# Kernel tuning notes

Hardware: AMD Instinct MI355X
Metric: run time of the kernel (lower is better)

Reference implementation:

```python
import jax, jax.numpy as jnp
import numpy as np

DECAY = 0.99
EPS = 1e-05


def setup_inputs() -> dict:
    key = jax.random.key(0)
    k1, k2, k3, k4 = jax.random.split(key, 4)
    x = jax.random.normal(k1, (32, 64, 64, 64), jnp.float32)          # [B,H,W,dim]
    embed = jax.random.normal(k2, (64, 1024), jnp.float32)            # [dim, n_embed] buffer
    cluster_size = jax.random.uniform(k3, (1024,), jnp.float32)       # EMA cluster-size buffer
    embed_avg = jax.random.normal(k4, (64, 1024), jnp.float32)        # EMA embed-avg buffer
    return {"x": x, "embed": embed, "cluster_size": cluster_size, "embed_avg": embed_avg}


def reference(x, embed, cluster_size, embed_avg):
    dim = x.shape[-1]
    n_embed = embed.shape[1]
    flatten = x.reshape(-1, dim)                                      # [N, dim]
    # squared distances: ||f||^2 - 2 f.E + ||e||^2   -> [N, n_embed]
    dist = ((flatten * flatten).sum(1, keepdims=True)
            - 2.0 * (flatten @ embed)
            + (embed * embed).sum(0, keepdims=True))
    idx = jnp.argmin(dist, axis=1)                                    # [N]
    quantize = jnp.take(embed.T, idx, axis=0).reshape(x.shape)        # codebook gather
    embed_ind = idx.reshape(x.shape[:-1])

    # EMA codebook update (training branch); stats detached as in torch (buffers, .data ops)
    fl = jax.lax.stop_gradient(flatten)
    onehot_sum = jax.ops.segment_sum(jnp.ones_like(idx, dtype=x.dtype), idx, num_segments=n_embed)
    embed_sum = jax.ops.segment_sum(fl, idx, num_segments=n_embed).T  # [dim, n_embed]
    new_cluster_size = DECAY * cluster_size + (1.0 - DECAY) * onehot_sum
    new_embed_avg = DECAY * embed_avg + (1.0 - DECAY) * embed_sum
    n = new_cluster_size.sum()
    cs = (new_cluster_size + EPS) / (n + n_embed * EPS) * n
    new_embed = new_embed_avg / cs[None, :]

    diff = jnp.mean((jax.lax.stop_gradient(quantize) - x) ** 2)       # commitment loss
    quantize_st = x + jax.lax.stop_gradient(quantize - x)             # straight-through
    return (quantize_st, diff, embed_ind, new_cluster_size, new_embed_avg, new_embed)
```

## Files before the change

kernel.cpp:

```cpp
#include <hip/hip_runtime.h>


#define N_ROWS 131072
#define DIM    64
#define NEMB   1024
#define NRANGE 32
#define KMASK  0xFFFFFC00u
#define TAUK   0.05f

static constexpr float DECAYF = 0.99f;
static constexpr float OMDF   = (float)(1.0 - 0.99);
static constexpr float EPSF   = 1e-5f;
static constexpr float NEPSF  = (float)(1024 * 1e-5);

typedef __attribute__((ext_vector_type(8))) short short8;
typedef __attribute__((ext_vector_type(4))) float f32x4;

static __device__ __forceinline__ unsigned short f2bf(float f) {
    unsigned int u = __builtin_bit_cast(unsigned int, f);
    unsigned int r = (u + 0x7FFFu + ((u >> 16) & 1u)) >> 16;
    return (unsigned short)r;
}
static __device__ __forceinline__ float bf2f(unsigned short h) {
    unsigned int u = ((unsigned int)h) << 16;
    return __builtin_bit_cast(float, u);
}

#define WS_ESUM    0
#define WS_CNTF    65536
#define WS_DIFF    66560
#define WS_FLAGCNT 66561
#define WS_N       66562
#define WS_EE      66564
#define WS_EMBEDT  67588
#define WS_IDX     133124
#define WS_FLAGLST 264196
#define WS_BFRAG   395268
#define WS_CNTPART 460804
#define WS_PART    493572
#define WS_NEED_BYTES ((size_t)(WS_PART + NRANGE * 65536) * 4)

__global__ void prep_kernel(const float* __restrict__ embed,
                            float* __restrict__ embedT,
                            float* __restrict__ ee,
                            uint4* __restrict__ BfragG,
                            float* __restrict__ ws_diff) {
    int tid = blockIdx.x * 256 + threadIdx.x;
    if (tid == 0) ws_diff[0] = 0.f;
    for (int i = 0; i < 4; ++i) {
        int id = i * 16384 + tid;
        int d = id >> 10, e = id & 1023;
        embedT[e * 64 + d] = embed[id];
    }
    if (tid < NEMB) {
        float s = 0.f;
        for (int d = 0; d < DIM; ++d) {
            float v = embed[d * 1024 + tid];
            s = fmaf(v, v, s);
        }
        ee[tid] = s;
    }
    int fid  = tid >> 6;
    int lane = tid & 63;
    int hl = fid & 1, kt = (fid >> 1) & 1, ct = fid >> 2;
    int col = ct * 16 + (lane & 15);
    int k0  = kt * 32 + (lane >> 4) * 8;
    unsigned short u[8];
    #pragma unroll
    for (int j = 0; j < 8; ++j) {
        float v = -2.0f * embed[(k0 + j) * 1024 + col];
        unsigned short h = f2bf(v);
        if (hl) h = f2bf(v - bf2f(h));
        u[j] = h;
    }
    uint4 wv;
    wv.x = (unsigned)u[0] | ((unsigned)u[1] << 16);
    wv.y = (unsigned)u[2] | ((unsigned)u[3] << 16);
    wv.z = (unsigned)u[4] | ((unsigned)u[5] << 16);
    wv.w = (unsigned)u[6] | ((unsigned)u[7] << 16);
    BfragG[fid * 64 + lane] = wv;
}

__global__ __launch_bounds__(256) void dist_kernel(
        const float* __restrict__ x, const uint4* __restrict__ BfragG,
        const float* __restrict__ ee, const float* __restrict__ embed,
        const float* __restrict__ embedT,
        float* __restrict__ out_q, float* __restrict__ out_ind,
        int* __restrict__ ws_idx, float* __restrict__ ws_diff) {
    __shared__ float sEE[1024];
    __shared__ int   sIdx[128];
    __shared__ float red[4];
    __shared__ int   sFlagCnt;
    __shared__ int   sFlagRows[128];
    __shared__ float sx[8][64];
    __shared__ float sff[8];
    __shared__ float sbdw[8][4];
    __shared__ int   sbiw[8][4];
    __shared__ int   schg[8];

    const int t = threadIdx.x;
    const int w = t >> 6, lane = t & 63;
    const int quad = lane >> 4, wl = lane & 15;
    const int rbase = blockIdx.x * 128;

    short8 a_hi[2][2], a_lo[2][2];
    #pragma unroll
    for (int rt = 0; rt < 2; ++rt) {
        int row = rbase + w * 32 + rt * 16 + wl;
        #pragma unroll
        for (int kt = 0; kt < 2; ++kt) {
            const float* px = x + (size_t)row * 64 + kt * 32 + quad * 8;
            float4 v0 = *(const float4*)px;
            float4 v1 = *(const float4*)(px + 4);
            float vv[8] = {v0.x, v0.y, v0.z, v0.w, v1.x, v1.y, v1.z, v1.w};
            short8 ah, al;
            #pragma unroll
            for (int j = 0; j < 8; ++j) {
                unsigned short h = f2bf(vv[j]);
                ah[j] = (short)h;
                al[j] = (short)f2bf(vv[j] - bf2f(h));
            }
            a_hi[rt][kt] = ah; a_lo[rt][kt] = al;
        }
    }

    for (int i = t; i < 1024; i += 256) sEE[i] = ee[i];
    if (t == 0) sFlagCnt = 0;

    float b1[8], b2[8];
    #pragma unroll
    for (int s = 0; s < 8; ++s) { b1[s] = 3.4e38f; b2[s] = 3.4e38f; }

    const f32x4 zacc = {0.f, 0.f, 0.f, 0.f};

    __syncthreads();

#define GBODY(CB0, CB1, CB2, CB3, COLV)                                        \
    {                                                                          \
        short8 bh0 = __builtin_bit_cast(short8, CB0);                          \
        short8 bl0 = __builtin_bit_cast(short8, CB1);                          \
        short8 bh1 = __builtin_bit_cast(short8, CB2);                          \
        short8 bl1 = __builtin_bit_cast(short8, CB3);                          \
        float eec = sEE[COLV];                                                 \
        unsigned colu = (unsigned)(COLV);                                      \
        _Pragma("unroll")                                                      \
        for (int rt = 0; rt < 2; ++rt) {                                       \
            f32x4 c0 = __builtin_amdgcn_mfma_f32_16x16x32_bf16(a_lo[rt][0], bh0, zacc, 0, 0, 0); \
            f32x4 c1 = __builtin_amdgcn_mfma_f32_16x16x32_bf16(a_lo[rt][1], bh1, zacc, 0, 0, 0); \
            c0 = __builtin_amdgcn_mfma_f32_16x16x32_bf16(a_hi[rt][0], bl0, c0, 0, 0, 0); \
            c1 = __builtin_amdgcn_mfma_f32_16x16x32_bf16(a_hi[rt][1], bl1, c1, 0, 0, 0); \
            c0 = __builtin_amdgcn_mfma_f32_16x16x32_bf16(a_hi[rt][0], bh0, c0, 0, 0, 0); \
            c1 = __builtin_amdgcn_mfma_f32_16x16x32_bf16(a_hi[rt][1], bh1, c1, 0, 0, 0); \
            _Pragma("unroll")                                                  \
            for (int reg = 0; reg < 4; ++reg) {                                \
                float s = c0[reg] + c1[reg] + eec;                             \
                unsigned ku = ((__builtin_bit_cast(unsigned, s) + 0x200u) & KMASK) | colu; \
                float key = __builtin_bit_cast(float, ku);                     \
                int st = rt * 4 + reg;                                         \
                b2[st] = __builtin_amdgcn_fmed3f(key, b1[st], b2[st]);         \
                b1[st] = fminf(key, b1[st]);                                   \
            }                                                                  \
        }                                                                      \
    }

#define LOADB(S0, S1, S2, S3, P)                                               \
    { const uint4* _p = (P); S0 = _p[0]; S1 = _p[64]; S2 = _p[128]; S3 = _p[192]; }

    {
        const uint4* pa = BfragG + lane;
        uint4 A0, A1, A2, A3, B0, B1, B2, B3;
        uint4 C0, C1, C2, C3, D0, D1, D2, D3;
        LOADB(A0, A1, A2, A3, pa);
        LOADB(B0, B1, B2, B3, pa + 256);
        LOADB(C0, C1, C2, C3, pa + 512);
        LOADB(D0, D1, D2, D3, pa + 768);
        int col = wl;
        for (int it = 0; it < 64; it += 4) {
            GBODY(A0, A1, A2, A3, col);
            if (it + 4 < 64) LOADB(A0, A1, A2, A3, pa + (it + 4) * 256);
            GBODY(B0, B1, B2, B3, col + 16);
            if (it + 5 < 64) LOADB(B0, B1, B2, B3, pa + (it + 5) * 256);
            GBODY(C0, C1, C2, C3, col + 32);
            if (it + 6 < 64) LOADB(C0, C1, C2, C3, pa + (it + 6) * 256);
            GBODY(D0, D1, D2, D3, col + 48);
            if (it + 7 < 64) LOADB(D0, D1, D2, D3, pa + (it + 7) * 256);
            col += 64;
        }
    }
#undef GBODY
#undef LOADB

    for (int m = 1; m < 16; m <<= 1) {
        #pragma unroll
        for (int s = 0; s < 8; ++s) {
            float o1 = __shfl_xor(b1[s], m);
            float o2 = __shfl_xor(b2[s], m);
            float mx = fmaxf(b1[s], o1);
            b1[s] = fminf(b1[s], o1);
            b2[s] = fminf(fminf(b2[s], o2), mx);
        }
    }
    if (wl == 0) {
        #pragma unroll
        for (int s = 0; s < 8; ++s) {
            int rt = s >> 2, reg = s & 3;
            int rloc = w * 32 + rt * 16 + quad * 4 + reg;
            int row = rbase + rloc;
            unsigned kb = __builtin_bit_cast(unsigned, b1[s]);
            int col = (int)(kb & 1023u);
            sIdx[rloc] = col;
            ws_idx[row] = col;
            out_ind[row] = (float)col;
            float v1 = __builtin_bit_cast(float, kb & KMASK);
            float v2 = __builtin_bit_cast(float, __builtin_bit_cast(unsigned, b2[s]) & KMASK);
            if (v2 - v1 < TAUK) {
                int p = atomicAdd(&sFlagCnt, 1);
                sFlagRows[p] = rloc;
            }
        }
    }
    __syncthreads();

    {
        int r = t >> 1, hh = t & 1;
        int e = sIdx[r];
        const float4* et = (const float4*)(embedT + e * 64 + hh * 32);
        const float4* xr = (const float4*)(x + (size_t)(rbase + r) * 64 + hh * 32);
        float4*       qo = (float4*)(out_q + (size_t)(rbase + r) * 64 + hh * 32);
        float dsum = 0.f;
        #pragma unroll
        for (int v = 0; v < 8; ++v) {
            float4 q4 = et[v];
            float4 x4 = xr[v];
            float dx = q4.x - x4.x, dy = q4.y - x4.y, dz = q4.z - x4.z, dw = q4.w - x4.w;
            float4 o;
            o.x = x4.x + dx; o.y = x4.y + dy; o.z = x4.z + dz; o.w = x4.w + dw;
            qo[v] = o;
            dsum += dx * dx + dy * dy + dz * dz + dw * dw;
        }
        for (int o2 = 32; o2 > 0; o2 >>= 1) dsum += __shfl_down(dsum, o2);
        if (lane == 0) red[w] = dsum;
        __syncthreads();
        if (t == 0) atomicAdd(ws_diff, red[0] + red[1] + red[2] + red[3]);
    }

    __syncthreads();
    int fcnt = sFlagCnt;
    for (int base = 0; base < fcnt; base += 8) {
        int nr = fcnt - base; if (nr > 8) nr = 8;
        __syncthreads();
        for (int l = t; l < nr * 64; l += 256) {
            int rl = sFlagRows[base + (l >> 6)];
            sx[l >> 6][l & 63] = x[(size_t)(rbase + rl) * 64 + (l & 63)];
        }
        __syncthreads();
        if (t < nr) {
            float ff = 0.f;
            for (int k = 0; k < 64; ++k) ff = fmaf(sx[t][k], sx[t][k], ff);
            sff[t] = ff;
        }
        float acc[8][4];
        #pragma unroll
        for (int r = 0; r < 8; ++r)
            #pragma unroll
            for (int j = 0; j < 4; ++j) acc[r][j] = 0.f;
        int c0i = t * 4;
        for (int k = 0; k < 64; ++k) {
            float4 e4 = *(const float4*)(embed + k * 1024 + c0i);
            #pragma unroll
            for (int r = 0; r < 8; ++r) {
                float xk = sx[r][k];
                acc[r][0] = fmaf(xk, e4.x, acc[r][0]);
                acc[r][1] = fmaf(xk, e4.y, acc[r][1]);
                acc[r][2] = fmaf(xk, e4.z, acc[r][2]);
                acc[r][3] = fmaf(xk, e4.w, acc[r][3]);
            }
        }
        __syncthreads();
        #pragma unroll
        for (int r = 0; r < 8; ++r) {
            if (r < nr) {
                float ff = sff[r];
                float bd = 3.4e38f; int bi = 0;
                #pragma unroll
                for (int j = 0; j < 4; ++j) {
                    float d = (ff - 2.f * acc[r][j]) + sEE[c0i + j];
                    if (d < bd) { bd = d; bi = c0i + j; }
                }
                for (int m = 32; m > 0; m >>= 1) {
                    float od = __shfl_xor(bd, m);
                    int   oi = __shfl_xor(bi, m);
                    if (od < bd || (od == bd && oi < bi)) { bd = od; bi = oi; }
                }
                if (lane == 0) { sbdw[r][w] = bd; sbiw[r][w] = bi; }
            }
        }
        __syncthreads();
        if (t < nr) {
            float bd = sbdw[t][0]; int bi = sbiw[t][0];
            #pragma unroll
            for (int k2 = 1; k2 < 4; ++k2) {
                float od = sbdw[t][k2]; int oi = sbiw[t][k2];
                if (od < bd || (od == bd && oi < bi)) { bd = od; bi = oi; }
            }
            int rl = sFlagRows[base + t];
            int oi_ = sIdx[rl];
            schg[t] = (bi != oi_) ? bi : -1;
            if (bi != oi_) {
                ws_idx[rbase + rl] = bi;
                out_ind[rbase + rl] = (float)bi;
            }
        }
        __syncthreads();
        for (int r = w; r < nr; r += 4) {
            int ni = schg[r];
            if (ni >= 0) {
                int rl = sFlagRows[base + r];
                int row = rbase + rl;
                int oi_ = sIdx[rl];
                float xv = sx[r][lane];
                float dn   = embedT[ni * 64 + lane] - xv;
                float dold = embedT[oi_ * 64 + lane] - xv;
                out_q[(size_t)row * 64 + lane] = xv + dn;
                float delta = dn * dn - dold * dold;
                for (int o = 32; o > 0; o >>= 1) delta += __shfl_down(delta, o);
                if (lane == 0) atomicAdd(ws_diff, delta);
            }
        }
    }
}

__global__ __launch_bounds__(1024) void scatter_kernel(
        const int* __restrict__ idx, const float* __restrict__ x,
        float* __restrict__ part_or_esum, float* __restrict__ cntp_or_cntf,
        int use_atomic) {
    __shared__ float shist[8192];
    __shared__ float scnt[1024];
    const int t = threadIdx.x;
    const int bid = blockIdx.x;
    const int oct = (bid >> 3) & 7;
    const int rb  = (bid & 7) | ((bid >> 6) << 3);
    const int sid = rb * 8 + oct;
    const int w = t >> 6, lane = t & 63;
    const int g = lane >> 3, d = lane & 7;

    for (int i = t; i < 8192; i += 1024) shist[i] = 0.f;
    if (oct == 0) { if (t < 1024) scnt[t] = 0.f; }
    __syncthreads();

    const int row0 = rb * 4096 + w * 256;
    int rcur = row0 + g;
    int e_n = idx[rcur];
    float x_n = x[(size_t)rcur * 64 + oct * 8 + d];
    for (int it = 0; it < 32; ++it) {
        int e = e_n; float xv = x_n;
        int rnext = rcur + 8;
        if (it < 31) {
            e_n = idx[rnext];
            x_n = x[(size_t)rnext * 64 + oct * 8 + d];
        }
        rcur = rnext;
        atomicAdd(&shist[e * 8 + d], xv);
        if (oct == 0 && d == 0) atomicAdd(&scnt[e], 1.0f);
    }
    __syncthreads();

    if (!use_atomic) {
        float* dst = part_or_esum + (size_t)sid * 8192;
        for (int out = t; out < 8192; out += 1024)
            dst[out] = shist[(out & 1023) * 8 + (out >> 10)];
        if (oct == 0) {
            float* cdst = cntp_or_cntf + rb * 1024;
            if (t < 1024) cdst[t] = scnt[t];
        }
    } else {
        for (int out = t; out < 8192; out += 1024) {
            float v = shist[(out & 1023) * 8 + (out >> 10)];
            if (v != 0.f)
                atomicAdd(&part_or_esum[(oct * 8 + (out >> 10)) * 1024 + (out & 1023)], v);
        }
        if (oct == 0) {
            if (t < 1024) {
                float c = scnt[t];
                if (c != 0.f) atomicAdd(&cntp_or_cntf[t], c);
            }
        }
    }
}

__global__ __launch_bounds__(1024) void finalizeF(
        const float* __restrict__ cluster_size, const float* __restrict__ cntp,
        const float* __restrict__ part, int nrb,
        const float* __restrict__ ws_diff, const float* __restrict__ embed_avg,
        float* __restrict__ out_diff, float* __restrict__ out_ncs,
        float* __restrict__ out_nea, float* __restrict__ out_ne) {
    __shared__ float sred[16];
    __shared__ float sn;
    const int tid = threadIdx.x;
    const int b = blockIdx.x;
    float c = 0.f;
    for (int k = 0; k < nrb; ++k) c += cntp[k * 1024 + tid];
    float ncs = DECAYF * cluster_size[tid] + OMDF * c;
    float v = ncs;
    for (int o = 32; o > 0; o >>= 1) v += __shfl_down(v, o);
    if ((tid & 63) == 0) sred[tid >> 6] = v;
    __syncthreads();
    if (tid == 0) {
        float n = 0.f;
        for (int i = 0; i < 16; ++i) n += sred[i];
        sn = n;
        if (b == 0) out_diff[0] = ws_diff[0] * (1.0f / 8388608.0f);
    }
    __syncthreads();
    float n = sn;
    if (b == 0) out_ncs[tid] = ncs;
    int j = b * 1024 + tid;
    float es = 0.f;
    for (int k = 0; k < nrb; ++k) es += part[(size_t)k * 65536 + j];
    float nea = DECAYF * embed_avg[j] + OMDF * es;
    out_nea[j] = nea;
    float cs = (ncs + EPSF) / (n + NEPSF) * n;
    out_ne[j] = nea / cs;
}

extern "C" void kernel_launch(void* const* d_in, const int* in_sizes, int n_in,
                              void* d_out, int out_size, void* d_ws, size_t ws_size,
                              hipStream_t stream) {
    const float* x            = (const float*)d_in[0];
    const float* embed        = (const float*)d_in[1];
    const float* cluster_size = (const float*)d_in[2];
    const float* embed_avg    = (const float*)d_in[3];

    float* out = (float*)d_out;
    float* out_q    = out;
    float* out_diff = out + 8388608;
    float* out_ind  = out + 8388609;
    float* out_ncs  = out + 8519681;
    float* out_nea  = out + 8520705;
    float* out_ne   = out + 8586241;

    float* ws = (float*)d_ws;
    float* ws_esum     = ws + WS_ESUM;
    float* ws_cntf     = ws + WS_CNTF;
    float* ws_diff     = ws + WS_DIFF;
    float* ws_ee       = ws + WS_EE;
    float* ws_embedT   = ws + WS_EMBEDT;
    int*   ws_idx      = (int*)(ws + WS_IDX);
    uint4* ws_Bfrag    = (uint4*)(ws + WS_BFRAG);
    float* ws_cntpart  = ws + WS_CNTPART;
    float* ws_part     = ws + WS_PART;

    const int use_part = (ws_size >= WS_NEED_BYTES) ? 1 : 0;

    if (!use_part) {
        hipMemsetAsync(d_ws, 0, (size_t)(WS_FLAGCNT + 1) * 4, stream);
    }

    prep_kernel<<<64, 256, 0, stream>>>(embed, ws_embedT, ws_ee, ws_Bfrag, ws_diff);
    dist_kernel<<<N_ROWS / 128, 256, 0, stream>>>(x, ws_Bfrag, ws_ee, embed,
                                                  ws_embedT, out_q, out_ind,
                                                  ws_idx, ws_diff);
    scatter_kernel<<<NRANGE * 8, 1024, 0, stream>>>(
        ws_idx, x,
        use_part ? ws_part : ws_esum,
        use_part ? ws_cntpart : ws_cntf,
        use_part ? 0 : 1);
    finalizeF<<<64, 1024, 0, stream>>>(cluster_size,
                                       use_part ? ws_cntpart : ws_cntf,
                                       use_part ? ws_part : ws_esum,
                                       use_part ? NRANGE : 1,
                                       ws_diff, embed_avg,
                                       out_diff, out_ncs, out_nea, out_ne);
}
```

Measured before the change: 248.6 us.

## Fuse scatter and finalize via last-blocks ticket barrier; tweak argmin key rounding

Merges the scatter kernel and the finalize kernel into one launch. Each block takes a ticket from an atomic counter after writing its partial histograms, and the last 64 blocks spin until all 256 have finished, then do the EMA finalize. This removes one kernel launch and its gap. The change also drops the +0x200 rounding in the packed argmin key and raises the TAUK threshold, which changes how many rows fall into the exact-recheck path. The spin-wait assumes all 256 blocks can be resident at once, and the key change may alter tie and near-tie behaviour.

```diff
diff --git a/kernel.cpp b/kernel.cpp
--- a/kernel.cpp
+++ b/kernel.cpp
@@ -6,7 +6,7 @@
 #define NEMB   1024
 #define NRANGE 32
 #define KMASK  0xFFFFFC00u
-#define TAUK   0.05f
+#define TAUK   0.07f
 
 static constexpr float DECAYF = 0.99f;
 static constexpr float OMDF   = (float)(1.0 - 0.99);
@@ -25,11 +25,14 @@
     unsigned int u = ((unsigned int)h) << 16;
     return __builtin_bit_cast(float, u);
 }
+static __device__ __forceinline__ float agent_ld(const float* p) {
+    return __hip_atomic_load(p, __ATOMIC_RELAXED, __HIP_MEMORY_SCOPE_AGENT);
+}
 
 #define WS_ESUM    0
 #define WS_CNTF    65536
 #define WS_DIFF    66560
-#define WS_FLAGCNT 66561
+#define WS_DONE    66561
 #define WS_N       66562
 #define WS_EE      66564
 #define WS_EMBEDT  67588
@@ -44,9 +47,10 @@
                             float* __restrict__ embedT,
                             float* __restrict__ ee,
                             uint4* __restrict__ BfragG,
-                            float* __restrict__ ws_diff) {
+                            float* __restrict__ ws_diff,
+                            int* __restrict__ ws_done) {
     int tid = blockIdx.x * 256 + threadIdx.x;
-    if (tid == 0) ws_diff[0] = 0.f;
+    if (tid == 0) { ws_diff[0] = 0.f; ws_done[0] = 0; }
     for (int i = 0; i < 4; ++i) {
         int id = i * 16384 + tid;
         int d = id >> 10, e = id & 1023;
@@ -154,7 +158,7 @@
             _Pragma("unroll")                                                  \
             for (int reg = 0; reg < 4; ++reg) {                                \
                 float s = c0[reg] + c1[reg] + eec;                             \
-                unsigned ku = ((__builtin_bit_cast(unsigned, s) + 0x200u) & KMASK) | colu; \
+                unsigned ku = (__builtin_bit_cast(unsigned, s) & KMASK) | colu;\
                 float key = __builtin_bit_cast(float, ku);                     \
                 int st = rt * 4 + reg;                                         \
                 b2[st] = __builtin_amdgcn_fmed3f(key, b1[st], b2[st]);         \
@@ -330,12 +334,20 @@
     }
 }
 
-__global__ __launch_bounds__(1024) void scatter_kernel(
+__global__ __launch_bounds__(1024) void scatter_fin(
         const int* __restrict__ idx, const float* __restrict__ x,
-        float* __restrict__ part_or_esum, float* __restrict__ cntp_or_cntf,
-        int use_atomic) {
+        float* __restrict__ part, float* __restrict__ cntp,
+        const float* __restrict__ cluster_size,
+        const float* __restrict__ ws_diff,
+        const float* __restrict__ embed_avg,
+        float* __restrict__ out_diff, float* __restrict__ out_ncs,
+        float* __restrict__ out_nea, float* __restrict__ out_ne,
+        int* __restrict__ done) {
     __shared__ float shist[8192];
     __shared__ float scnt[1024];
+    __shared__ float sred[16];
+    __shared__ float sn;
+    __shared__ int   sTicket;
     const int t = threadIdx.x;
     const int bid = blockIdx.x;
     const int oct = (bid >> 3) & 7;
@@ -365,25 +377,98 @@
     }
     __syncthreads();
 
-    if (!use_atomic) {
-        float* dst = part_or_esum + (size_t)sid * 8192;
+    {
+        float* dst = part + (size_t)sid * 8192;
         for (int out = t; out < 8192; out += 1024)
             dst[out] = shist[(out & 1023) * 8 + (out >> 10)];
         if (oct == 0) {
-            float* cdst = cntp_or_cntf + rb * 1024;
+            float* cdst = cntp + rb * 1024;
             if (t < 1024) cdst[t] = scnt[t];
         }
-    } else {
-        for (int out = t; out < 8192; out += 1024) {
-            float v = shist[(out & 1023) * 8 + (out >> 10)];
-            if (v != 0.f)
-                atomicAdd(&part_or_esum[(oct * 8 + (out >> 10)) * 1024 + (out & 1023)], v);
-        }
-        if (oct == 0) {
-            if (t < 1024) {
-                float c = scnt[t];
-                if (c != 0.f) atomicAdd(&cntp_or_cntf[t], c);
-            }
+    }
+
+    __threadfence();
+    __syncthreads();
+    if (t == 0) sTicket = atomicAdd(done, 1);
+    __syncthreads();
+    int ticket = sTicket;
+    if (ticket < 192) return;
+    int b = ticket - 192;
+    if (t == 0) {
+        while (atomicAdd(done, 0) < 256) { }
+    }
+    __syncthreads();
+    __threadfence();
+
+    {
+        float c = 0.f;
+        for (int k = 0; k < NRANGE; ++k) c += agent_ld(&cntp[k * 1024 + t]);
+        float ncs = DECAYF * cluster_size[t] + OMDF * c;
+        float v = ncs;
+        for (int o = 32; o > 0; o >>= 1) v += __shfl_down(v, o);
+        if ((t & 63) == 0) sred[t >> 6] = v;
+        __syncthreads();
+        if (t == 0) {
+            float n = 0.f;
+            for (int i = 0; i < 16; ++i) n += sred[i];
+            sn = n;
+            if (b == 0) out_diff[0] = ws_diff[0] * (1.0f / 8388608.0f);
+        }
+        __syncthreads();
+        float n = sn;
+        if (b == 0) out_ncs[t] = ncs;
+        int j = b * 1024 + t;
+        float es = 0.f;
+        for (int k = 0; k < NRANGE; ++k) es += agent_ld(&part[(size_t)k * 65536 + j]);
+        float nea = DECAYF * embed_avg[j] + OMDF * es;
+        out_nea[j] = nea;
+        float cs = (ncs + EPSF) / (n + NEPSF) * n;
+        out_ne[j] = nea / cs;
+    }
+}
+
+__global__ __launch_bounds__(1024) void scatter_kernel(
+        const int* __restrict__ idx, const float* __restrict__ x,
+        float* __restrict__ esum, float* __restrict__ cntf) {
+    __shared__ float shist[8192];
+    __shared__ float scnt[1024];
+    const int t = threadIdx.x;
+    const int bid = blockIdx.x;
+    const int oct = (bid >> 3) & 7;
+    const int rb  = (bid & 7) | ((bid >> 6) << 3);
+    const int w = t >> 6, lane = t & 63;
+    const int g = lane >> 3, d = lane & 7;
+
+    for (int i = t; i < 8192; i += 1024) shist[i] = 0.f;
+    if (oct == 0) { if (t < 1024) scnt[t] = 0.f; }
+    __syncthreads();
+
+    const int row0 = rb * 4096 + w * 256;
+    int rcur = row0 + g;
+    int e_n = idx[rcur];
+    float x_n = x[(size_t)rcur * 64 + oct * 8 + d];
+    for (int it = 0; it < 32; ++it) {
+        int e = e_n; float xv = x_n;
+        int rnext = rcur + 8;
+        if (it < 31) {
+            e_n = idx[rnext];
+            x_n = x[(size_t)rnext * 64 + oct * 8 + d];
+        }
+        rcur = rnext;
+        atomicAdd(&shist[e * 8 + d], xv);
+        if (oct == 0 && d == 0) atomicAdd(&scnt[e], 1.0f);
+    }
+    __syncthreads();
+
+    for (int out = t; out < 8192; out += 1024) {
+        float v = shist[(out & 1023) * 8 + (out >> 10)];
+        if (v != 0.f)
+            atomicAdd(&esum[(oct * 8 + (out >> 10)) * 1024 + (out & 1023)], v);
+    }
+    if (oct == 0) {
+        if (t < 1024) {
+            float c = scnt[t];
+            if (c != 0.f) atomicAdd(&cntf[t], c);
         }
     }
 }
@@ -443,6 +528,7 @@
     float* ws_esum     = ws + WS_ESUM;
     float* ws_cntf     = ws + WS_CNTF;
     float* ws_diff     = ws + WS_DIFF;
+    int*   ws_done     = (int*)(ws + WS_DONE);
     float* ws_ee       = ws + WS_EE;
     float* ws_embedT   = ws + WS_EMBEDT;
     int*   ws_idx      = (int*)(ws + WS_IDX);
@@ -453,22 +539,22 @@
     const int use_part = (ws_size >= WS_NEED_BYTES) ? 1 : 0;
 
     if (!use_part) {
-        hipMemsetAsync(d_ws, 0, (size_t)(WS_FLAGCNT + 1) * 4, stream);
-    }
-
-    prep_kernel<<<64, 256, 0, stream>>>(embed, ws_embedT, ws_ee, ws_Bfrag, ws_diff);
+        hipMemsetAsync(d_ws, 0, (size_t)(WS_DONE + 1) * 4, stream);
+    }
+
+    prep_kernel<<<64, 256, 0, stream>>>(embed, ws_embedT, ws_ee, ws_Bfrag,
+                                        ws_diff, ws_done);
     dist_kernel<<<N_ROWS / 128, 256, 0, stream>>>(x, ws_Bfrag, ws_ee, embed,
                                                   ws_embedT, out_q, out_ind,
                                                   ws_idx, ws_diff);
-    scatter_kernel<<<NRANGE * 8, 1024, 0, stream>>>(
-        ws_idx, x,
-        use_part ? ws_part : ws_esum,
-        use_part ? ws_cntpart : ws_cntf,
-        use_part ? 0 : 1);
-    finalizeF<<<64, 1024, 0, stream>>>(cluster_size,
-                                       use_part ? ws_cntpart : ws_cntf,
-                                       use_part ? ws_part : ws_esum,
-                                       use_part ? NRANGE : 1,
-                                       ws_diff, embed_avg,
-                                       out_diff, out_ncs, out_nea, out_ne);
-}
+    if (use_part) {
+        scatter_fin<<<NRANGE * 8, 1024, 0, stream>>>(
+            ws_idx, x, ws_part, ws_cntpart, cluster_size, ws_diff, embed_avg,
+            out_diff, out_ncs, out_nea, out_ne, ws_done);
+    } else {
+        scatter_kernel<<<NRANGE * 8, 1024, 0, stream>>>(ws_idx, x, ws_esum, ws_cntf);
+        finalizeF<<<64, 1024, 0, stream>>>(cluster_size, ws_cntf, ws_esum, 1,
+                                           ws_diff, embed_avg,
+                                           out_diff, out_ncs, out_nea, out_ne);
+    }
+}
```

Result: slower. 369.7 us (+48.7%).
